# Kernel tuning notes

Measured on AMD Instinct MI355X. Metric: run time of the kernel, lower is better.

## Reference

```python
import jax, jax.numpy as jnp
import numpy as np

B, N, C, E, K, L = 8, 20000, 256, 320000, 3, 2
EPS = 1e-5

def setup_inputs() -> dict:
    key = jax.random.key(0)
    ks = jax.random.split(key, 8)
    features = jax.random.normal(ks[0], (B * N, C), dtype=jnp.float32)
    edge_index = jax.random.randint(ks[1], (2, E), 0, N, dtype=jnp.int64)
    # ChebConv params per layer: K linear weights [C,C] (no per-lin bias) + one bias [C]
    W = jax.random.normal(ks[2], (L, K, C, C), dtype=jnp.float32) * 0.05
    b = jax.random.normal(ks[3], (L, C), dtype=jnp.float32) * 0.05
    # node-mode LayerNorm affine params per layer
    ln_w = jnp.ones((L, C), dtype=jnp.float32)
    ln_b = jnp.zeros((L, C), dtype=jnp.float32)
    return {"features": features, "W": W, "b": b, "ln_w": ln_w, "ln_b": ln_b,
            "edge_index": edge_index, "batch_size": B}


def reference(features, W, b, ln_w, ln_b, edge_index, batch_size):
    n = features.shape[0] // batch_size
    c = features.shape[-1]
    src, dst = edge_index[0], edge_index[1]
    # sym-normalized Laplacian, lambda_max=2: L_hat = 2L/lmax - I = -D^-1/2 A D^-1/2
    deg = jax.ops.segment_sum(jnp.ones_like(src, dtype=features.dtype), src, num_segments=n)
    dis = jnp.where(deg > 0, jax.lax.rsqrt(jnp.where(deg > 0, deg, 1.0)), 0.0)
    norm = -dis[src] * dis[dst]  # [E]
    n_layers, k_order = W.shape[0], W.shape[1]

    def prop(x):  # L_hat @ x via gather-scale-scatter
        return jax.ops.segment_sum(norm[:, None] * x[src], dst, num_segments=n)

    def cheb(x, Wl, bl):
        Tx0 = x
        out = Tx0 @ Wl[0]
        Tx1 = prop(Tx0)
        out = out + Tx1 @ Wl[1]
        for k in range(2, k_order):
            Tx2 = 2.0 * prop(Tx1) - Tx0
            out = out + Tx2 @ Wl[k]
            Tx0, Tx1 = Tx1, Tx2
        return out + bl

    def single(feats):  # [n, c] -> [n, c]
        x = feats
        for i in range(n_layers):
            # NOTE: module passes original features to every layer's conv (faithful)
            x = cheb(feats, W[i], b[i])
            mu = jnp.mean(x, axis=-1, keepdims=True)
            var = jnp.var(x, axis=-1, keepdims=True)
            x = (x - mu) * jax.lax.rsqrt(var + EPS) * ln_w[i] + ln_b[i]
            # dropout p=0.0 -> identity
        return x

    fb = features.reshape(batch_size, n, c)
    return jax.vmap(single)(fb)
```

## Files before the change

### kernel.cpp

```cpp
#include <hip/hip_runtime.h>
#include <stdint.h>

#define BB 8
#define NN 20000
#define CC 256
#define EE 320000
#define KK 3
#define MROWS (BB * NN)
#define ROWU (BB * CC)

__device__ __forceinline__ float bf2f(ushort u) {
    union { uint32_t ui; float f; } v; v.ui = ((uint32_t)u) << 16; return v.f;
}
__device__ __forceinline__ ushort f2bf(float f) {
    union { uint32_t ui; float f; } v; v.f = f;
    uint32_t r = (v.ui + 0x7FFFu + ((v.ui >> 16) & 1u)) >> 16;
    return (ushort)r;
}

typedef __bf16 bf16x8 __attribute__((ext_vector_type(8)));
typedef float  f32x4  __attribute__((ext_vector_type(4)));

__device__ __forceinline__ void gload16(const void* gptr, void* lptr) {
    __builtin_amdgcn_global_load_lds(
        (const __attribute__((address_space(1))) void*)gptr,
        (__attribute__((address_space(3))) void*)lptr, 16, 0, 0);
}

__global__ void detect_k(const int* __restrict__ raw, int* __restrict__ flag) {
    int i = blockIdx.x * 256 + threadIdx.x;
    int v = 0;
    int idx = 2 * i + 1;
    if (i < EE) v = raw[idx];
    unsigned long long m = __ballot(v != 0);
    if ((threadIdx.x & 63) == 0 && m) atomicOr(flag, 1);
}

__global__ void convcount_k(const int* __restrict__ raw, const int* __restrict__ flag,
                            int mode,
                            int* __restrict__ src, int* __restrict__ dst,
                            int* __restrict__ deg_out, int* __restrict__ cnt_in) {
    int e = blockIdx.x * 256 + threadIdx.x;
    if (e >= EE) return;
    int m = mode ? mode : (*flag ? 1 : 2);
    int s, d;
    if (m == 2) { s = raw[2 * e]; d = raw[2 * EE + 2 * e]; }
    else        { s = raw[e];     d = raw[EE + e]; }
    src[e] = s; dst[e] = d;
    atomicAdd(&deg_out[s], 1);
    atomicAdd(&cnt_in[d], 1);
}

__global__ void __launch_bounds__(1024) scan_k(const int* __restrict__ cnt_in,
                                               const int* __restrict__ deg_out,
                                               int* __restrict__ row_ptr,
                                               float* __restrict__ dis) {
    __shared__ int wpart[16];
    const int t = threadIdx.x;
    const int lane = t & 63, wid = t >> 6;
    const int base = t * 20;
    int local[20];
    int sum = 0;
#pragma unroll
    for (int i = 0; i < 20; i++) {
        int idx = base + i;
        int v = (idx < NN) ? cnt_in[idx] : 0;
        local[i] = sum;
        sum += v;
    }
    int sc = sum;
#pragma unroll
    for (int off = 1; off < 64; off <<= 1) {
        int u = __shfl_up(sc, off, 64);
        if (lane >= off) sc += u;
    }
    if (lane == 63) wpart[wid] = sc;
    __syncthreads();
    if (wid == 0 && lane < 16) {
        int v = wpart[lane];
#pragma unroll
        for (int off = 1; off < 16; off <<= 1) {
            int u = __shfl_up(v, off, 64);
            if (lane >= off) v += u;
        }
        wpart[lane] = v;
    }
    __syncthreads();
    int wbase = (wid > 0) ? wpart[wid - 1] : 0;
    int tbase = wbase + sc - sum;
#pragma unroll
    for (int i = 0; i < 20; i++) {
        int idx = base + i;
        if (idx < NN) row_ptr[idx] = tbase + local[i];
    }
    if (t == 1023) row_ptr[NN] = tbase + sum;
    for (int i = t; i < NN; i += 1024) {
        int d = deg_out[i];
        dis[i] = (d > 0) ? rsqrtf((float)d) : 0.0f;
    }
}

__global__ void fill_k(const int* __restrict__ src, const int* __restrict__ dst,
                       const int* __restrict__ row_ptr, int* __restrict__ fillc,
                       const float* __restrict__ dis,
                       int* __restrict__ col, float* __restrict__ w) {
    int e = blockIdx.x * 256 + threadIdx.x;
    if (e >= EE) return;
    int s = src[e], d = dst[e];
    int pos = row_ptr[d] + atomicAdd(&fillc[d], 1);
    col[pos] = s;
    w[pos] = -dis[s] * dis[d];
}

__global__ void cvtwprep_k(const float* __restrict__ x, ushort* __restrict__ y,
                           const float* __restrict__ W, ushort* __restrict__ wt) {
    int bid = blockIdx.x;
    if (bid < MROWS * CC / 1024) {
        size_t idx = ((size_t)bid * 256 + threadIdx.x) * 4;
        int row = (int)(idx >> 8);
        int c = (int)(idx & 255);
        int b = row / NN, n = row - b * NN;
        float4 v = *(const float4*)(x + idx);
        ushort4 o = make_ushort4(f2bf(v.x), f2bf(v.y), f2bf(v.z), f2bf(v.w));
        *(ushort4*)(y + ((size_t)(n * BB + b) * CC + c)) = o;
    } else {
        int idx = (bid - MROWS * CC / 1024) * 256 + threadIdx.x;
        if (idx >= 256 * 768) return;
        int n = idx / 768, k = idx % 768;
        int sel = k >> 8, kk = k & 255;
        const float* W1 = W + KK * CC * CC;
        float v;
        if (sel == 0)      v = W1[kk * CC + n] - W1[2 * CC * CC + kk * CC + n];
        else if (sel == 1) v = W1[CC * CC + kk * CC + n];
        else               v = 2.0f * W1[2 * CC * CC + kk * CC + n];
        wt[idx] = f2bf(v);
    }
}

__global__ void __launch_bounds__(256) prop_k(const ushort* __restrict__ x,
                                              ushort* __restrict__ y,
                                              const int* __restrict__ row_ptr,
                                              const int* __restrict__ col,
                                              const float* __restrict__ w) {
    const int n = blockIdx.x;
    const int t = threadIdx.x;
    const int beg = row_ptr[n], end = row_ptr[n + 1];
    const ushort* xb = x + t * 8;
    float a0 = 0, a1 = 0, a2 = 0, a3 = 0, a4 = 0, a5 = 0, a6 = 0, a7 = 0;
    int j = beg;
    for (; j + 4 <= end; j += 4) {
        int s0 = col[j], s1 = col[j + 1], s2 = col[j + 2], s3 = col[j + 3];
        float w0 = w[j], w1 = w[j + 1], w2 = w[j + 2], w3 = w[j + 3];
        uint4 v0 = *(const uint4*)(xb + (size_t)s0 * ROWU);
        uint4 v1 = *(const uint4*)(xb + (size_t)s1 * ROWU);
        uint4 v2 = *(const uint4*)(xb + (size_t)s2 * ROWU);
        uint4 v3 = *(const uint4*)(xb + (size_t)s3 * ROWU);
        a0 += w0 * bf2f((ushort)v0.x) + w1 * bf2f((ushort)v1.x) + w2 * bf2f((ushort)v2.x) + w3 * bf2f((ushort)v3.x);
        a1 += w0 * bf2f((ushort)(v0.x >> 16)) + w1 * bf2f((ushort)(v1.x >> 16)) + w2 * bf2f((ushort)(v2.x >> 16)) + w3 * bf2f((ushort)(v3.x >> 16));
        a2 += w0 * bf2f((ushort)v0.y) + w1 * bf2f((ushort)v1.y) + w2 * bf2f((ushort)v2.y) + w3 * bf2f((ushort)v3.y);
        a3 += w0 * bf2f((ushort)(v0.y >> 16)) + w1 * bf2f((ushort)(v1.y >> 16)) + w2 * bf2f((ushort)(v2.y >> 16)) + w3 * bf2f((ushort)(v3.y >> 16));
        a4 += w0 * bf2f((ushort)v0.z) + w1 * bf2f((ushort)v1.z) + w2 * bf2f((ushort)v2.z) + w3 * bf2f((ushort)v3.z);
        a5 += w0 * bf2f((ushort)(v0.z >> 16)) + w1 * bf2f((ushort)(v1.z >> 16)) + w2 * bf2f((ushort)(v2.z >> 16)) + w3 * bf2f((ushort)(v3.z >> 16));
        a6 += w0 * bf2f((ushort)v0.w) + w1 * bf2f((ushort)v1.w) + w2 * bf2f((ushort)v2.w) + w3 * bf2f((ushort)v3.w);
        a7 += w0 * bf2f((ushort)(v0.w >> 16)) + w1 * bf2f((ushort)(v1.w >> 16)) + w2 * bf2f((ushort)(v2.w >> 16)) + w3 * bf2f((ushort)(v3.w >> 16));
    }
    for (; j < end; j++) {
        int s = col[j];
        float wt = w[j];
        uint4 v = *(const uint4*)(xb + (size_t)s * ROWU);
        a0 += wt * bf2f((ushort)v.x);
        a1 += wt * bf2f((ushort)(v.x >> 16));
        a2 += wt * bf2f((ushort)v.y);
        a3 += wt * bf2f((ushort)(v.y >> 16));
        a4 += wt * bf2f((ushort)v.z);
        a5 += wt * bf2f((ushort)(v.z >> 16));
        a6 += wt * bf2f((ushort)v.w);
        a7 += wt * bf2f((ushort)(v.w >> 16));
    }
    uint4 o;
    o.x = (uint32_t)f2bf(a0) | ((uint32_t)f2bf(a1) << 16);
    o.y = (uint32_t)f2bf(a2) | ((uint32_t)f2bf(a3) << 16);
    o.z = (uint32_t)f2bf(a4) | ((uint32_t)f2bf(a5) << 16);
    o.w = (uint32_t)f2bf(a6) | ((uint32_t)f2bf(a7) << 16);
    *(uint4*)(y + (size_t)n * ROWU + t * 8) = o;
}

__global__ void __launch_bounds__(512, 4) gemmln_k(const ushort* __restrict__ a0,
                                                   const ushort* __restrict__ a1,
                                                   const ushort* __restrict__ a2,
                                                   const ushort* __restrict__ wt,
                                                   const float* __restrict__ bias,
                                                   const float* __restrict__ lnw,
                                                   const float* __restrict__ lnb,
                                                   float* __restrict__ out) {
    __shared__ ushort As[128 * 64];
    __shared__ ushort Bs[256 * 64];
    __shared__ float reds[128][4];
    __shared__ float redq[128][4];
    const int tid = threadIdx.x;
    const int wid = tid >> 6, lane = tid & 63;
    const int wrow = wid >> 2, wcol = wid & 3;
    const int quad = lane >> 4, l16 = lane & 15;
    const int row0 = blockIdx.x * 128;

    f32x4 acc[4][4] = {};

    for (int kt = 0; kt < 12; kt++) {
        const ushort* ab = (kt < 4) ? a0 : ((kt < 8) ? a1 : a2);
        const int kl = (kt & 3) * 64;
        const int kg = kt * 64;
        __syncthreads();
#pragma unroll
        for (int q2 = 0; q2 < 2; q2++) {
            int c = q2 * 512 + tid;
            int m = c >> 3, p = c & 7;
            int kq = (p ^ (m & 7)) * 8;
            gload16(ab + (size_t)(row0 + m) * CC + kl + kq,
                    &As[(q2 * 512 + wid * 64) * 8]);
        }
#pragma unroll
        for (int q2 = 0; q2 < 4; q2++) {
            int c = q2 * 512 + tid;
            int m = c >> 3, p = c & 7;
            int kq = (p ^ (m & 7)) * 8;
            gload16(wt + (size_t)m * 768 + kg + kq,
                    &Bs[(q2 * 512 + wid * 64) * 8]);
        }
        __syncthreads();

#pragma unroll
        for (int ks = 0; ks < 2; ks++) {
            bf16x8 af[4], bfr[4];
#pragma unroll
            for (int mt = 0; mt < 4; mt++) {
                int r = wrow * 64 + mt * 16 + l16;
                int pc = (ks * 4 + quad) ^ (r & 7);
                af[mt] = *(const bf16x8*)&As[r * 64 + pc * 8];
            }
#pragma unroll
            for (int nt = 0; nt < 4; nt++) {
                int r = wcol * 64 + nt * 16 + l16;
                int pc = (ks * 4 + quad) ^ (r & 7);
                bfr[nt] = *(const bf16x8*)&Bs[r * 64 + pc * 8];
            }
#pragma unroll
            for (int mt = 0; mt < 4; mt++)
#pragma unroll
                for (int nt = 0; nt < 4; nt++)
                    acc[mt][nt] = __builtin_amdgcn_mfma_f32_16x16x32_bf16(
                        af[mt], bfr[nt], acc[mt][nt], 0, 0, 0);
        }
    }

    float bv[4], lwv[4], lbv[4];
#pragma unroll
    for (int nt = 0; nt < 4; nt++) {
        int c = wcol * 64 + nt * 16 + l16;
        bv[nt] = bias[c]; lwv[nt] = lnw[c]; lbv[nt] = lnb[c];
    }
#pragma unroll
    for (int mt = 0; mt < 4; mt++) {
#pragma unroll
        for (int r = 0; r < 4; r++) {
            float s = 0.0f, q = 0.0f;
#pragma unroll
            for (int nt = 0; nt < 4; nt++) {
                float v = acc[mt][nt][r] + bv[nt];
                s += v; q += v * v;
            }
#pragma unroll
            for (int off = 1; off < 16; off <<= 1) {
                s += __shfl_xor(s, off, 64);
                q += __shfl_xor(q, off, 64);
            }
            if (l16 == 0) {
                int ml = wrow * 64 + mt * 16 + quad * 4 + r;
                reds[ml][wcol] = s;
                redq[ml][wcol] = q;
            }
        }
    }
    __syncthreads();
#pragma unroll
    for (int mt = 0; mt < 4; mt++) {
#pragma unroll
        for (int r = 0; r < 4; r++) {
            int ml = wrow * 64 + mt * 16 + quad * 4 + r;
            float s = reds[ml][0] + reds[ml][1] + reds[ml][2] + reds[ml][3];
            float q = redq[ml][0] + redq[ml][1] + redq[ml][2] + redq[ml][3];
            float mean = s * (1.0f / CC);
            float var = q * (1.0f / CC) - mean * mean;
            float rs = rsqrtf(var + 1e-5f);
            int m = row0 + ml;
            int n = m >> 3, b = m & 7;
            size_t orow = (size_t)b * NN + n;
#pragma unroll
            for (int nt = 0; nt < 4; nt++) {
                int c = wcol * 64 + nt * 16 + l16;
                float v = (acc[mt][nt][r] + bv[nt] - mean) * rs * lwv[nt] + lbv[nt];
                out[orow * CC + c] = v;
            }
        }
    }
}

extern "C" void kernel_launch(void* const* d_in, const int* in_sizes, int n_in,
                              void* d_out, int out_size, void* d_ws, size_t ws_size,
                              hipStream_t stream) {
    const float* feats = (const float*)d_in[0];
    const float* W     = (const float*)d_in[1];
    const float* bvec  = (const float*)d_in[2];
    const float* lnw   = (const float*)d_in[3];
    const float* lnb   = (const float*)d_in[4];
    const int*   eidx  = (const int*)d_in[5];
    float* outp = (float*)d_out;

    int* flag    = (int*)d_ws;
    int* deg_out = flag + 64;
    int* cnt_in  = deg_out + NN;
    int* fillc   = cnt_in + NN;
    int* row_ptr = fillc + NN;
    int* srcw    = row_ptr + (NN + 64);
    int* dstw    = srcw + EE;
    int* colw    = dstw + EE;
    float* disw  = (float*)(colw + EE);
    float* ww    = disw + (NN + 64);
    uintptr_t bf_base = ((uintptr_t)(ww + EE) + 255) & ~(uintptr_t)255;
    ushort* featsb = (ushort*)bf_base;
    ushort* tx1b   = featsb + (size_t)MROWS * CC;
    ushort* p2b    = tx1b + (size_t)MROWS * CC;
    ushort* wcat   = p2b + (size_t)MROWS * CC;

    hipMemsetAsync(flag, 0, (size_t)(64 + 3 * NN) * sizeof(int), stream);

    int mode = 0;
    long long esz = in_sizes ? (long long)in_sizes[5] : 0;
    if (esz == (long long)2 * EE * 8) mode = 2;
    else if (esz == (long long)2 * EE * 4) mode = 1;

    int eb = (EE + 255) / 256;
    if (mode == 0) detect_k<<<eb, 256, 0, stream>>>(eidx, flag);
    convcount_k<<<eb, 256, 0, stream>>>(eidx, flag, mode, srcw, dstw, deg_out, cnt_in);
    scan_k<<<1, 1024, 0, stream>>>(cnt_in, deg_out, row_ptr, disw);
    fill_k<<<eb, 256, 0, stream>>>(srcw, dstw, row_ptr, fillc, disw, colw, ww);

    cvtwprep_k<<<MROWS * CC / 1024 + 768, 256, 0, stream>>>(feats, featsb, W, wcat);

    prop_k<<<NN, 256, 0, stream>>>(featsb, tx1b, row_ptr, colw, ww);
    prop_k<<<NN, 256, 0, stream>>>(tx1b, p2b, row_ptr, colw, ww);

    gemmln_k<<<MROWS / 128, 512, 0, stream>>>(featsb, tx1b, p2b, wcat,
                                              bvec + CC, lnw + CC, lnb + CC, outp);
}
```

Before: 907.5 us.

## Double-buffer GEMM K-tiles and pack CSR column/weight into int2

The fused GEMM+LayerNorm kernel now loads K-tiles of 32 into two LDS buffers, prefetching the next tile while MFMAs run on the current one, with one barrier per step instead of two. The XOR swizzle on the LDS layout is dropped. Separately, CSR column indices and edge weights are stored interleaved as int2, so each edge in the propagation kernel needs one 8-byte load instead of two scalar loads. The narrower tiles double the number of loop iterations and barriers, and the unswizzled 64-byte LDS rows may cause bank conflicts on fragment reads.

```diff
diff --git a/kernel.cpp b/kernel.cpp
--- a/kernel.cpp
+++ b/kernel.cpp
@@ -103,13 +103,12 @@
 __global__ void fill_k(const int* __restrict__ src, const int* __restrict__ dst,
                        const int* __restrict__ row_ptr, int* __restrict__ fillc,
                        const float* __restrict__ dis,
-                       int* __restrict__ col, float* __restrict__ w) {
+                       int2* __restrict__ cw) {
     int e = blockIdx.x * 256 + threadIdx.x;
     if (e >= EE) return;
     int s = src[e], d = dst[e];
     int pos = row_ptr[d] + atomicAdd(&fillc[d], 1);
-    col[pos] = s;
-    w[pos] = -dis[s] * dis[d];
+    cw[pos] = make_int2(s, __float_as_int(-dis[s] * dis[d]));
 }
 
 __global__ void cvtwprep_k(const float* __restrict__ x, ushort* __restrict__ y,
@@ -140,8 +139,7 @@
 __global__ void __launch_bounds__(256) prop_k(const ushort* __restrict__ x,
                                               ushort* __restrict__ y,
                                               const int* __restrict__ row_ptr,
-                                              const int* __restrict__ col,
-                                              const float* __restrict__ w) {
+                                              const int2* __restrict__ cw) {
     const int n = blockIdx.x;
     const int t = threadIdx.x;
     const int beg = row_ptr[n], end = row_ptr[n + 1];
@@ -149,8 +147,10 @@
     float a0 = 0, a1 = 0, a2 = 0, a3 = 0, a4 = 0, a5 = 0, a6 = 0, a7 = 0;
     int j = beg;
     for (; j + 4 <= end; j += 4) {
-        int s0 = col[j], s1 = col[j + 1], s2 = col[j + 2], s3 = col[j + 3];
-        float w0 = w[j], w1 = w[j + 1], w2 = w[j + 2], w3 = w[j + 3];
+        int2 e0 = cw[j], e1 = cw[j + 1], e2 = cw[j + 2], e3 = cw[j + 3];
+        int s0 = e0.x, s1 = e1.x, s2 = e2.x, s3 = e3.x;
+        float w0 = __int_as_float(e0.y), w1 = __int_as_float(e1.y);
+        float w2 = __int_as_float(e2.y), w3 = __int_as_float(e3.y);
         uint4 v0 = *(const uint4*)(xb + (size_t)s0 * ROWU);
         uint4 v1 = *(const uint4*)(xb + (size_t)s1 * ROWU);
         uint4 v2 = *(const uint4*)(xb + (size_t)s2 * ROWU);
@@ -165,8 +165,9 @@
         a7 += w0 * bf2f((ushort)(v0.w >> 16)) + w1 * bf2f((ushort)(v1.w >> 16)) + w2 * bf2f((ushort)(v2.w >> 16)) + w3 * bf2f((ushort)(v3.w >> 16));
     }
     for (; j < end; j++) {
-        int s = col[j];
-        float wt = w[j];
+        int2 e0 = cw[j];
+        int s = e0.x;
+        float wt = __int_as_float(e0.y);
         uint4 v = *(const uint4*)(xb + (size_t)s * ROWU);
         a0 += wt * bf2f((ushort)v.x);
         a1 += wt * bf2f((ushort)(v.x >> 16));
@@ -185,6 +186,18 @@
     *(uint4*)(y + (size_t)n * ROWU + t * 8) = o;
 }
 
+#define STAGE(buf, kt_) do {                                                   \
+    const ushort* ab_ = ((kt_) < 8) ? a0 : (((kt_) < 16) ? a1 : a2);           \
+    const int kl_ = ((kt_) & 7) * 32;                                          \
+    const int kg_ = (kt_) * 32;                                                \
+    gload16(ab_ + (size_t)(row0 + (tid >> 2)) * CC + kl_ + (tid & 3) * 8,      \
+            &As[buf][wid * 512]);                                              \
+    gload16(wt + (size_t)(tid >> 2) * 768 + kg_ + (tid & 3) * 8,               \
+            &Bs[buf][wid * 512]);                                              \
+    gload16(wt + (size_t)((512 + tid) >> 2) * 768 + kg_ + (tid & 3) * 8,       \
+            &Bs[buf][4096 + wid * 512]);                                       \
+} while (0)
+
 __global__ void __launch_bounds__(512, 4) gemmln_k(const ushort* __restrict__ a0,
                                                    const ushort* __restrict__ a1,
                                                    const ushort* __restrict__ a2,
@@ -193,8 +206,8 @@
                                                    const float* __restrict__ lnw,
                                                    const float* __restrict__ lnb,
                                                    float* __restrict__ out) {
-    __shared__ ushort As[128 * 64];
-    __shared__ ushort Bs[256 * 64];
+    __shared__ ushort As[2][128 * 32];
+    __shared__ ushort Bs[2][256 * 32];
     __shared__ float reds[128][4];
     __shared__ float redq[128][4];
     const int tid = threadIdx.x;
@@ -205,51 +218,28 @@
 
     f32x4 acc[4][4] = {};
 
-    for (int kt = 0; kt < 12; kt++) {
-        const ushort* ab = (kt < 4) ? a0 : ((kt < 8) ? a1 : a2);
-        const int kl = (kt & 3) * 64;
-        const int kg = kt * 64;
+    STAGE(0, 0);
+    __syncthreads();
+    int cur = 0;
+    for (int kt = 0; kt < 24; kt++) {
+        if (kt < 23) STAGE(cur ^ 1, kt + 1);
+
+        bf16x8 af[4], bfr[4];
+#pragma unroll
+        for (int mt = 0; mt < 4; mt++)
+            af[mt] = *(const bf16x8*)&As[cur][(wrow * 64 + mt * 16 + l16) * 32 + quad * 8];
+#pragma unroll
+        for (int nt = 0; nt < 4; nt++)
+            bfr[nt] = *(const bf16x8*)&Bs[cur][(wcol * 64 + nt * 16 + l16) * 32 + quad * 8];
+#pragma unroll
+        for (int mt = 0; mt < 4; mt++)
+#pragma unroll
+            for (int nt = 0; nt < 4; nt++)
+                acc[mt][nt] = __builtin_amdgcn_mfma_f32_16x16x32_bf16(
+                    af[mt], bfr[nt], acc[mt][nt], 0, 0, 0);
+
         __syncthreads();
-#pragma unroll
-        for (int q2 = 0; q2 < 2; q2++) {
-            int c = q2 * 512 + tid;
-            int m = c >> 3, p = c & 7;
-            int kq = (p ^ (m & 7)) * 8;
-            gload16(ab + (size_t)(row0 + m) * CC + kl + kq,
-                    &As[(q2 * 512 + wid * 64) * 8]);
-        }
-#pragma unroll
-        for (int q2 = 0; q2 < 4; q2++) {
-            int c = q2 * 512 + tid;
-            int m = c >> 3, p = c & 7;
-            int kq = (p ^ (m & 7)) * 8;
-            gload16(wt + (size_t)m * 768 + kg + kq,
-                    &Bs[(q2 * 512 + wid * 64) * 8]);
-        }
-        __syncthreads();
-
-#pragma unroll
-        for (int ks = 0; ks < 2; ks++) {
-            bf16x8 af[4], bfr[4];
-#pragma unroll
-            for (int mt = 0; mt < 4; mt++) {
-                int r = wrow * 64 + mt * 16 + l16;
-                int pc = (ks * 4 + quad) ^ (r & 7);
-                af[mt] = *(const bf16x8*)&As[r * 64 + pc * 8];
-            }
-#pragma unroll
-            for (int nt = 0; nt < 4; nt++) {
-                int r = wcol * 64 + nt * 16 + l16;
-                int pc = (ks * 4 + quad) ^ (r & 7);
-                bfr[nt] = *(const bf16x8*)&Bs[r * 64 + pc * 8];
-            }
-#pragma unroll
-            for (int mt = 0; mt < 4; mt++)
-#pragma unroll
-                for (int nt = 0; nt < 4; nt++)
-                    acc[mt][nt] = __builtin_amdgcn_mfma_f32_16x16x32_bf16(
-                        af[mt], bfr[nt], acc[mt][nt], 0, 0, 0);
-        }
+        cur ^= 1;
     }
 
     float bv[4], lwv[4], lbv[4];
@@ -322,10 +312,9 @@
     int* row_ptr = fillc + NN;
     int* srcw    = row_ptr + (NN + 64);
     int* dstw    = srcw + EE;
-    int* colw    = dstw + EE;
-    float* disw  = (float*)(colw + EE);
-    float* ww    = disw + (NN + 64);
-    uintptr_t bf_base = ((uintptr_t)(ww + EE) + 255) & ~(uintptr_t)255;
+    int2* cw     = (int2*)(dstw + EE);
+    float* disw  = (float*)(cw + EE);
+    uintptr_t bf_base = ((uintptr_t)(disw + NN + 64) + 255) & ~(uintptr_t)255;
     ushort* featsb = (ushort*)bf_base;
     ushort* tx1b   = featsb + (size_t)MROWS * CC;
     ushort* p2b    = tx1b + (size_t)MROWS * CC;
@@ -342,12 +331,12 @@
     if (mode == 0) detect_k<<<eb, 256, 0, stream>>>(eidx, flag);
     convcount_k<<<eb, 256, 0, stream>>>(eidx, flag, mode, srcw, dstw, deg_out, cnt_in);
     scan_k<<<1, 1024, 0, stream>>>(cnt_in, deg_out, row_ptr, disw);
-    fill_k<<<eb, 256, 0, stream>>>(srcw, dstw, row_ptr, fillc, disw, colw, ww);
+    fill_k<<<eb, 256, 0, stream>>>(srcw, dstw, row_ptr, fillc, disw, cw);
 
     cvtwprep_k<<<MROWS * CC / 1024 + 768, 256, 0, stream>>>(feats, featsb, W, wcat);
 
-    prop_k<<<NN, 256, 0, stream>>>(featsb, tx1b, row_ptr, colw, ww);
-    prop_k<<<NN, 256, 0, stream>>>(tx1b, p2b, row_ptr, colw, ww);
+    prop_k<<<NN, 256, 0, stream>>>(featsb, tx1b, row_ptr, cw);
+    prop_k<<<NN, 256, 0, stream>>>(tx1b, p2b, row_ptr, cw);
 
     gemmln_k<<<MROWS / 128, 512, 0, stream>>>(featsb, tx1b, p2b, wcat,
                                               bvec + CC, lnw + CC, lnb + CC, outp);
```

Measured after the change: 911.2 us. About the same (+0.4%).
